# Optimization experiments

Hardware: AMD Instinct MI355X
Metric: run time of the kernel (lower is better)

## Reference

```python
import jax, jax.numpy as jnp
import numpy as np

DECAY = 0.25
THRESH = 0.4
TIME_WINDOW = 8


def act_fun(x):
    # Heaviside spike (forward of torch ActFun)
    return (x > 0.0).astype(x.dtype)


def setup_inputs() -> dict:
    key = jax.random.key(0)
    ks = jax.random.split(key, 12)
    B, C, H, W, T = 200, 2, 34, 34, TIME_WINDOW
    in_dim, h1, h2 = 2312, 800, 10
    return {
        "input": jax.random.normal(ks[0], (B, C, H, W, T), dtype=jnp.float32),
        "hebb1": jnp.zeros((in_dim, h1), dtype=jnp.float32),
        "hebb2": jnp.zeros((h1, h2), dtype=jnp.float32),
        "W1": jax.random.normal(ks[1], (h1, in_dim), dtype=jnp.float32) / np.sqrt(in_dim),
        "b1": jax.random.normal(ks[2], (h1,), dtype=jnp.float32) * 0.01,
        "W2": jax.random.normal(ks[3], (h2, h1), dtype=jnp.float32) / np.sqrt(h1),
        "b2": jax.random.normal(ks[4], (h2,), dtype=jnp.float32) * 0.01,
        "alpha1": 0.01 * jnp.ones((1,), dtype=jnp.float32),
        "alpha2": 0.01 * jnp.ones((1,), dtype=jnp.float32),
        "beta1": 0.01 * jax.random.uniform(ks[5], (1, in_dim), dtype=jnp.float32),
        "beta2": 0.01 * jax.random.uniform(ks[6], (1, h1), dtype=jnp.float32),
        "eta1": 0.1 * jax.random.uniform(ks[7], (1, h1), dtype=jnp.float32),
        "eta2": 0.1 * jax.random.uniform(ks[8], (1, h2), dtype=jnp.float32),
    }


def _mem_update(W, b, alpha, beta, eta, x, spike, mem, hebb, batch):
    # fc(x) + alpha * x @ hebb
    state = x @ W.T + b + alpha * (x @ hebb)
    mem = mem * (1.0 - spike) * DECAY + state
    now_spike = act_fun(mem - THRESH)
    # bmm of outer products then mean over batch == single GEMM / batch
    pre = x * jnp.clip(beta, 0.0, None)              # [B, in]
    post = mem / THRESH - eta                        # [B, out]
    hebb = 0.99 * hebb - (pre.T @ post) / batch      # [in, out]
    hebb = jnp.clip(hebb, -5.0, 5.0)
    return mem, now_spike, hebb


def reference(input, hebb1, hebb2, W1, b1, W2, b2, alpha1, alpha2, beta1, beta2, eta1, eta2):
    B = input.shape[0]
    T = input.shape[-1]
    xs = jnp.moveaxis(input, -1, 0).reshape(T, B, -1)  # [T, B, 2312]
    h1 = W1.shape[0]
    h2 = W2.shape[0]
    init = (
        jnp.zeros((B, h1), jnp.float32), jnp.zeros((B, h1), jnp.float32),
        jnp.zeros((B, h2), jnp.float32), jnp.zeros((B, h2), jnp.float32),
        hebb1, hebb2,
    )

    def step(carry, x):
        h1_mem, h1_spike, h2_mem, h2_spike, hb1, hb2 = carry
        h1_mem, h1_spike, hb1 = _mem_update(W1, b1, alpha1, beta1, eta1, x, h1_spike, h1_mem, hb1, B)
        h2_mem, h2_spike, hb2 = _mem_update(W2, b2, alpha2, beta2, eta2, h1_spike, h2_spike, h2_mem, hb2, B)
        return (h1_mem, h1_spike, h2_mem, h2_spike, hb1, hb2), None

    (h1_mem, h1_spike, h2_mem, h2_spike, hb1, hb2), _ = jax.lax.scan(step, init, xs)
    outs = h2_mem / THRESH
    return outs, hb1, hb2
```

## Files before the change

### kernel.cpp

```cpp
#include <hip/hip_runtime.h>

#define BATCH  200
#define IN_DIM 2312
#define HD1    800
#define HD2    10
#define TWIN   8
#define NSPLIT 8
#define KCH    304

__global__ __launch_bounds__(512) void k_transpose_in(const float* __restrict__ in,
                                                      float* __restrict__ xall) {
  __shared__ float lds[512];
  int b  = blockIdx.y;
  int i0 = blockIdx.x * 64;
  int tid = threadIdx.x;
  int il = tid >> 3, t = tid & 7;
  int i = i0 + il;
  lds[tid] = (i < IN_DIM) ? in[((size_t)(b * IN_DIM + i) << 3) + t] : 0.f;
  __syncthreads();
  int t2 = tid >> 6, il2 = tid & 63;
  int i2 = i0 + il2;
  if (i2 < IN_DIM)
    xall[((size_t)(t2 * BATCH + b)) * IN_DIM + i2] = lds[il2 * 8 + t2];
}

__global__ __launch_bounds__(256) void k_init(const float* __restrict__ h1in,
                                              const float* __restrict__ h2in,
                                              float* __restrict__ hebb1,
                                              float* __restrict__ hebb2,
                                              float* __restrict__ mem1,
                                              float* __restrict__ spike1,
                                              float* __restrict__ mem2,
                                              float* __restrict__ spike2) {
  int stride = gridDim.x * blockDim.x;
  int n1 = IN_DIM * HD1;
  for (int k = blockIdx.x * blockDim.x + threadIdx.x; k < n1; k += stride) {
    hebb1[k] = h1in[k];
    if (k < HD1 * HD2)  hebb2[k] = h2in[k];
    if (k < BATCH * HD1) { mem1[k] = 0.f; spike1[k] = 0.f; }
    if (k < BATCH * HD2) { mem2[k] = 0.f; spike2[k] = 0.f; }
  }
}

__global__ __launch_bounds__(256) void k_prep_wc1(const float* __restrict__ W1,
                                                  const float* __restrict__ hebb1,
                                                  const float* __restrict__ alpha1,
                                                  float* __restrict__ Wc1) {
  __shared__ float lds[32][33];
  float al = alpha1[0];
  int i0 = blockIdx.x * 32;
  int j0 = blockIdx.y * 32;
  int tx = threadIdx.x, ty = threadIdx.y;
#pragma unroll
  for (int q = 0; q < 4; q++) {
    int j = j0 + ty + q * 8, i = i0 + tx;
    lds[ty + q * 8][tx] = (j < HD1 && i < IN_DIM) ? W1[(size_t)j * IN_DIM + i] : 0.f;
  }
  __syncthreads();
#pragma unroll
  for (int q = 0; q < 4; q++) {
    int i = i0 + ty + q * 8, j = j0 + tx;
    if (i < IN_DIM)
      Wc1[(size_t)i * HD1 + j] = lds[tx][ty + q * 8] + al * hebb1[(size_t)i * HD1 + j];
  }
}

__global__ __launch_bounds__(256) void k_state_gemm(const float* __restrict__ xt,
                                                    const float* __restrict__ Wc1,
                                                    float* __restrict__ part) {
  __shared__ __align__(16) float As[16][68];
  __shared__ __align__(16) float Bs[16][68];
  int m0 = blockIdx.x * 64;
  int n0 = blockIdx.y * 64;
  int s  = blockIdx.z;
  int kstart = s * KCH;
  int kend   = (kstart + KCH < IN_DIM) ? kstart + KCH : IN_DIM;
  int tid = threadIdx.x;
  int tx = tid & 15, ty = tid >> 4;
  int a_m = tid >> 2;
  int a_k = (tid & 3) * 4;
  int b_k = tid >> 4;
  int b_n = (tid & 15) * 4;
  float acc[4][4] = {};
  for (int k0 = kstart; k0 < kend; k0 += 16) {
    float4 av = make_float4(0.f, 0.f, 0.f, 0.f);
    if (m0 + a_m < BATCH && k0 + a_k < kend)
      av = *(const float4*)&xt[(size_t)(m0 + a_m) * IN_DIM + k0 + a_k];
    As[a_k + 0][a_m] = av.x;
    As[a_k + 1][a_m] = av.y;
    As[a_k + 2][a_m] = av.z;
    As[a_k + 3][a_m] = av.w;
    float4 bv = make_float4(0.f, 0.f, 0.f, 0.f);
    if (k0 + b_k < kend && n0 + b_n < HD1)
      bv = *(const float4*)&Wc1[(size_t)(k0 + b_k) * HD1 + n0 + b_n];
    *(float4*)&Bs[b_k][b_n] = bv;
    __syncthreads();
#pragma unroll
    for (int kk = 0; kk < 16; kk++) {
      float4 a = *(const float4*)&As[kk][ty * 4];
      float4 b = *(const float4*)&Bs[kk][tx * 4];
      acc[0][0] += a.x * b.x; acc[0][1] += a.x * b.y; acc[0][2] += a.x * b.z; acc[0][3] += a.x * b.w;
      acc[1][0] += a.y * b.x; acc[1][1] += a.y * b.y; acc[1][2] += a.y * b.z; acc[1][3] += a.y * b.w;
      acc[2][0] += a.z * b.x; acc[2][1] += a.z * b.y; acc[2][2] += a.z * b.z; acc[2][3] += a.z * b.w;
      acc[3][0] += a.w * b.x; acc[3][1] += a.w * b.y; acc[3][2] += a.w * b.z; acc[3][3] += a.w * b.w;
    }
    __syncthreads();
  }
  int n_base = n0 + tx * 4;
  if (n_base < HD1) {
    float* pp = part + (size_t)s * BATCH * HD1;
#pragma unroll
    for (int dm = 0; dm < 4; dm++) {
      int m = m0 + ty * 4 + dm;
      if (m < BATCH)
        *(float4*)&pp[(size_t)m * HD1 + n_base] =
            make_float4(acc[dm][0], acc[dm][1], acc[dm][2], acc[dm][3]);
    }
  }
}

__global__ __launch_bounds__(256) void k_state_epi(const float* __restrict__ part,
                                                   const float* __restrict__ b1,
                                                   const float* __restrict__ eta1,
                                                   float* __restrict__ mem1,
                                                   float* __restrict__ spike1,
                                                   float* __restrict__ post1) {
  int g = blockIdx.x * blockDim.x + threadIdx.x;
  if (g >= BATCH * (HD1 / 4)) return;
  int m  = g / (HD1 / 4);
  int n4 = (g % (HD1 / 4)) * 4;
  size_t idx = (size_t)m * HD1 + n4;
  float4 sum = *(const float4*)&part[idx];
#pragma unroll
  for (int s = 1; s < NSPLIT; s++) {
    float4 p = *(const float4*)&part[(size_t)s * BATCH * HD1 + idx];
    sum.x += p.x; sum.y += p.y; sum.z += p.z; sum.w += p.w;
  }
  float4 bb = *(const float4*)&b1[n4];
  float4 ee = *(const float4*)&eta1[n4];
  float4 mo = *(const float4*)&mem1[idx];
  float4 so = *(const float4*)&spike1[idx];
  float st[4] = {sum.x + bb.x, sum.y + bb.y, sum.z + bb.z, sum.w + bb.w};
  float mof[4] = {mo.x, mo.y, mo.z, mo.w};
  float sof[4] = {so.x, so.y, so.z, so.w};
  float eef[4] = {ee.x, ee.y, ee.z, ee.w};
  float mn[4], sp[4], po[4];
#pragma unroll
  for (int q = 0; q < 4; q++) {
    mn[q] = mof[q] * (1.f - sof[q]) * 0.25f + st[q];
    sp[q] = (mn[q] - 0.4f > 0.f) ? 1.f : 0.f;
    po[q] = mn[q] / 0.4f - eef[q];
  }
  *(float4*)&mem1[idx]   = make_float4(mn[0], mn[1], mn[2], mn[3]);
  *(float4*)&spike1[idx] = make_float4(sp[0], sp[1], sp[2], sp[3]);
  *(float4*)&post1[idx]  = make_float4(po[0], po[1], po[2], po[3]);
}

__global__ __launch_bounds__(256) void k_hebb1(const float* __restrict__ xt,
                                               const float* __restrict__ post1,
                                               const float* __restrict__ beta1,
                                               float* __restrict__ hebb1) {
  __shared__ __align__(16) float As[16][68];
  __shared__ __align__(16) float Bs[16][68];
  int i0 = blockIdx.x * 64;
  int j0 = blockIdx.y * 64;
  int tid = threadIdx.x;
  int tx = tid & 15, ty = tid >> 4;
  int l_b = tid >> 4;
  int l_c = (tid & 15) * 4;
  float acc[4][4] = {};
  for (int b0 = 0; b0 < BATCH; b0 += 16) {
    float4 av = make_float4(0.f, 0.f, 0.f, 0.f);
    if (b0 + l_b < BATCH && i0 + l_c < IN_DIM)
      av = *(const float4*)&xt[(size_t)(b0 + l_b) * IN_DIM + i0 + l_c];
    *(float4*)&As[l_b][l_c] = av;
    float4 bv = make_float4(0.f, 0.f, 0.f, 0.f);
    if (b0 + l_b < BATCH && j0 + l_c < HD1)
      bv = *(const float4*)&post1[(size_t)(b0 + l_b) * HD1 + j0 + l_c];
    *(float4*)&Bs[l_b][l_c] = bv;
    __syncthreads();
#pragma unroll
    for (int kk = 0; kk < 16; kk++) {
      float4 a = *(const float4*)&As[kk][ty * 4];
      float4 b = *(const float4*)&Bs[kk][tx * 4];
      acc[0][0] += a.x * b.x; acc[0][1] += a.x * b.y; acc[0][2] += a.x * b.z; acc[0][3] += a.x * b.w;
      acc[1][0] += a.y * b.x; acc[1][1] += a.y * b.y; acc[1][2] += a.y * b.z; acc[1][3] += a.y * b.w;
      acc[2][0] += a.z * b.x; acc[2][1] += a.z * b.y; acc[2][2] += a.z * b.z; acc[2][3] += a.z * b.w;
      acc[3][0] += a.w * b.x; acc[3][1] += a.w * b.y; acc[3][2] += a.w * b.z; acc[3][3] += a.w * b.w;
    }
    __syncthreads();
  }
  int j_base = j0 + tx * 4;
  if (j_base < HD1) {
#pragma unroll
    for (int dm = 0; dm < 4; dm++) {
      int i = i0 + ty * 4 + dm;
      if (i >= IN_DIM) continue;
      float bc = fmaxf(beta1[i], 0.f);
      size_t idx = (size_t)i * HD1 + j_base;
      float4 h = *(const float4*)&hebb1[idx];
      float hv[4] = {h.x, h.y, h.z, h.w};
#pragma unroll
      for (int dn = 0; dn < 4; dn++) {
        float v = 0.99f * hv[dn] - bc * acc[dm][dn] * (1.f / 200.f);
        hv[dn] = fminf(fmaxf(v, -5.f), 5.f);
      }
      *(float4*)&hebb1[idx] = make_float4(hv[0], hv[1], hv[2], hv[3]);
    }
  }
}

__global__ __launch_bounds__(256) void k_layer2_state(const float* __restrict__ spike1,
                                                      const float* __restrict__ W2,
                                                      const float* __restrict__ b2,
                                                      const float* __restrict__ hebb2,
                                                      const float* __restrict__ alpha2,
                                                      const float* __restrict__ eta2,
                                                      float* __restrict__ mem2,
                                                      float* __restrict__ spike2,
                                                      float* __restrict__ post2,
                                                      float* __restrict__ outs) {
  int wid  = (int)((blockIdx.x * blockDim.x + threadIdx.x) >> 6);
  int lane = threadIdx.x & 63;
  if (wid >= BATCH * HD2) return;
  int b = wid / HD2, j = wid % HD2;
  float al = alpha2[0];
  float acc = 0.f;
  for (int i = lane; i < HD1; i += 64)
    acc += spike1[b * HD1 + i] * (W2[j * HD1 + i] + al * hebb2[i * HD2 + j]);
#pragma unroll
  for (int off = 32; off > 0; off >>= 1) acc += __shfl_down(acc, off, 64);
  if (lane == 0) {
    float state = acc + b2[j];
    int idx = b * HD2 + j;
    float mo = mem2[idx], so = spike2[idx];
    float mn = mo * (1.f - so) * 0.25f + state;
    mem2[idx]   = mn;
    spike2[idx] = (mn - 0.4f > 0.f) ? 1.f : 0.f;
    post2[idx]  = mn / 0.4f - eta2[j];
    outs[idx]   = mn / 0.4f;
  }
}

__global__ __launch_bounds__(256) void k_hebb2(const float* __restrict__ spike1,
                                               const float* __restrict__ post2,
                                               const float* __restrict__ beta2,
                                               float* __restrict__ hebb2) {
  int idx = blockIdx.x * blockDim.x + threadIdx.x;
  if (idx >= HD1 * HD2) return;
  int i = idx % HD1, j = idx / HD1;
  float acc = 0.f;
  for (int b = 0; b < BATCH; b++)
    acc += spike1[b * HD1 + i] * post2[b * HD2 + j];
  float bc = fmaxf(beta2[i], 0.f);
  float h = 0.99f * hebb2[i * HD2 + j] - bc * acc * (1.f / 200.f);
  hebb2[i * HD2 + j] = fminf(fmaxf(h, -5.f), 5.f);
}

extern "C" void kernel_launch(void* const* d_in, const int* in_sizes, int n_in,
                              void* d_out, int out_size, void* d_ws, size_t ws_size,
                              hipStream_t stream) {
  const float* input    = (const float*)d_in[0];
  const float* hebb1_in = (const float*)d_in[1];
  const float* hebb2_in = (const float*)d_in[2];
  const float* W1       = (const float*)d_in[3];
  const float* b1       = (const float*)d_in[4];
  const float* W2       = (const float*)d_in[5];
  const float* b2       = (const float*)d_in[6];
  const float* alpha1   = (const float*)d_in[7];
  const float* alpha2   = (const float*)d_in[8];
  const float* beta1    = (const float*)d_in[9];
  const float* beta2    = (const float*)d_in[10];
  const float* eta1     = (const float*)d_in[11];
  const float* eta2     = (const float*)d_in[12];

  float* out   = (float*)d_out;
  float* outs  = out;
  float* hebb1 = out + BATCH * HD2;
  float* hebb2 = hebb1 + (size_t)IN_DIM * HD1;

  float* ws     = (float*)d_ws;
  float* xall   = ws;
  float* Wc1    = xall + (size_t)TWIN * BATCH * IN_DIM;
  float* part   = Wc1 + (size_t)IN_DIM * HD1;
  float* mem1   = part + (size_t)NSPLIT * BATCH * HD1;
  float* spike1 = mem1 + BATCH * HD1;
  float* post1  = spike1 + BATCH * HD1;
  float* mem2   = post1 + BATCH * HD1;
  float* spike2 = mem2 + BATCH * HD2;
  float* post2  = spike2 + BATCH * HD2;

  k_transpose_in<<<dim3((IN_DIM + 63) / 64, BATCH), 512, 0, stream>>>(input, xall);
  k_init<<<1024, 256, 0, stream>>>(hebb1_in, hebb2_in, hebb1, hebb2,
                                   mem1, spike1, mem2, spike2);

  for (int t = 0; t < TWIN; t++) {
    const float* xt = xall + (size_t)t * BATCH * IN_DIM;
    k_prep_wc1<<<dim3(73, 25), dim3(32, 8), 0, stream>>>(W1, hebb1, alpha1, Wc1);
    k_state_gemm<<<dim3(4, 13, NSPLIT), 256, 0, stream>>>(xt, Wc1, part);
    k_state_epi<<<dim3((BATCH * (HD1 / 4) + 255) / 256), 256, 0, stream>>>(
        part, b1, eta1, mem1, spike1, post1);
    k_hebb1<<<dim3(37, 13), 256, 0, stream>>>(xt, post1, beta1, hebb1);
    k_layer2_state<<<dim3((BATCH * HD2 * 64 + 255) / 256), 256, 0, stream>>>(
        spike1, W2, b2, hebb2, alpha2, eta2, mem2, spike2, post2, outs);
    k_hebb2<<<dim3((HD1 * HD2 + 255) / 256), 256, 0, stream>>>(spike1, post2, beta2, hebb2);
  }
}
```

Before: 640.9 us.

## Hoist W1 transpose and fuse alpha*hebb1 combine into state GEMM loads

W1 is now transposed once before the time loop. The per-step kernel that built the combined weight Wc1 = W1^T + alpha*hebb1 is removed; the state GEMM instead reads W1T and hebb1 directly and combines them while loading its B tile. This drops one full-matrix write and read plus a launch per timestep. The GEMM and hebb1 kernels also move to 128 threads computing 8x4 outputs each, and the split-K factor rises to 16 with shorter K chunks. The trade-off is that hebb1 is re-read by each M block, and the epilogue now sums more partial buffers.

```diff
diff --git a/kernel.cpp b/kernel.cpp
--- a/kernel.cpp
+++ b/kernel.cpp
@@ -5,8 +5,8 @@
 #define HD1    800
 #define HD2    10
 #define TWIN   8
-#define NSPLIT 8
-#define KCH    304
+#define NSPLIT 16
+#define KCH    144
 
 __global__ __launch_bounds__(512) void k_transpose_in(const float* __restrict__ in,
                                                       float* __restrict__ xall) {
@@ -22,6 +22,26 @@
   int i2 = i0 + il2;
   if (i2 < IN_DIM)
     xall[((size_t)(t2 * BATCH + b)) * IN_DIM + i2] = lds[il2 * 8 + t2];
+}
+
+__global__ __launch_bounds__(256) void k_prep_w1t(const float* __restrict__ W1,
+                                                  float* __restrict__ W1T) {
+  __shared__ float lds[32][33];
+  int i0 = blockIdx.x * 32;
+  int j0 = blockIdx.y * 32;
+  int tx = threadIdx.x, ty = threadIdx.y;
+#pragma unroll
+  for (int q = 0; q < 4; q++) {
+    int j = j0 + ty + q * 8, i = i0 + tx;
+    lds[ty + q * 8][tx] = (j < HD1 && i < IN_DIM) ? W1[(size_t)j * IN_DIM + i] : 0.f;
+  }
+  __syncthreads();
+#pragma unroll
+  for (int q = 0; q < 4; q++) {
+    int i = i0 + ty + q * 8, j = j0 + tx;
+    if (i < IN_DIM)
+      W1T[(size_t)i * HD1 + j] = lds[tx][ty + q * 8];
+  }
 }
 
 __global__ __launch_bounds__(256) void k_init(const float* __restrict__ h1in,
@@ -42,31 +62,10 @@
   }
 }
 
-__global__ __launch_bounds__(256) void k_prep_wc1(const float* __restrict__ W1,
-                                                  const float* __restrict__ hebb1,
-                                                  const float* __restrict__ alpha1,
-                                                  float* __restrict__ Wc1) {
-  __shared__ float lds[32][33];
-  float al = alpha1[0];
-  int i0 = blockIdx.x * 32;
-  int j0 = blockIdx.y * 32;
-  int tx = threadIdx.x, ty = threadIdx.y;
-#pragma unroll
-  for (int q = 0; q < 4; q++) {
-    int j = j0 + ty + q * 8, i = i0 + tx;
-    lds[ty + q * 8][tx] = (j < HD1 && i < IN_DIM) ? W1[(size_t)j * IN_DIM + i] : 0.f;
-  }
-  __syncthreads();
-#pragma unroll
-  for (int q = 0; q < 4; q++) {
-    int i = i0 + ty + q * 8, j = j0 + tx;
-    if (i < IN_DIM)
-      Wc1[(size_t)i * HD1 + j] = lds[tx][ty + q * 8] + al * hebb1[(size_t)i * HD1 + j];
-  }
-}
-
-__global__ __launch_bounds__(256) void k_state_gemm(const float* __restrict__ xt,
-                                                    const float* __restrict__ Wc1,
+__global__ __launch_bounds__(128) void k_state_gemm(const float* __restrict__ xt,
+                                                    const float* __restrict__ W1T,
+                                                    const float* __restrict__ hebb1,
+                                                    const float* __restrict__ alpha1,
                                                     float* __restrict__ part) {
   __shared__ __align__(16) float As[16][68];
   __shared__ __align__(16) float Bs[16][68];
@@ -74,35 +73,57 @@
   int n0 = blockIdx.y * 64;
   int s  = blockIdx.z;
   int kstart = s * KCH;
-  int kend   = (kstart + KCH < IN_DIM) ? kstart + KCH : IN_DIM;
+  int kend   = (s == NSPLIT - 1) ? IN_DIM : kstart + KCH;
+  float al = alpha1[0];
   int tid = threadIdx.x;
   int tx = tid & 15, ty = tid >> 4;
   int a_m = tid >> 2;
   int a_k = (tid & 3) * 4;
-  int b_k = tid >> 4;
-  int b_n = (tid & 15) * 4;
-  float acc[4][4] = {};
+  int b_k = tid >> 3;
+  int b_n = (tid & 7) * 8;
+  float acc[8][4] = {};
   for (int k0 = kstart; k0 < kend; k0 += 16) {
-    float4 av = make_float4(0.f, 0.f, 0.f, 0.f);
-    if (m0 + a_m < BATCH && k0 + a_k < kend)
-      av = *(const float4*)&xt[(size_t)(m0 + a_m) * IN_DIM + k0 + a_k];
-    As[a_k + 0][a_m] = av.x;
-    As[a_k + 1][a_m] = av.y;
-    As[a_k + 2][a_m] = av.z;
-    As[a_k + 3][a_m] = av.w;
-    float4 bv = make_float4(0.f, 0.f, 0.f, 0.f);
-    if (k0 + b_k < kend && n0 + b_n < HD1)
-      bv = *(const float4*)&Wc1[(size_t)(k0 + b_k) * HD1 + n0 + b_n];
-    *(float4*)&Bs[b_k][b_n] = bv;
+#pragma unroll
+    for (int h = 0; h < 2; h++) {
+      int m = m0 + a_m + h * 32;
+      float4 av = make_float4(0.f, 0.f, 0.f, 0.f);
+      if (m < BATCH && k0 + a_k < kend)
+        av = *(const float4*)&xt[(size_t)m * IN_DIM + k0 + a_k];
+      As[a_k + 0][a_m + h * 32] = av.x;
+      As[a_k + 1][a_m + h * 32] = av.y;
+      As[a_k + 2][a_m + h * 32] = av.z;
+      As[a_k + 3][a_m + h * 32] = av.w;
+    }
+    {
+      int kb = k0 + b_k;
+      bool kv = (kb < kend);
+      size_t base = (size_t)kb * HD1 + n0 + b_n;
+#pragma unroll
+      for (int h = 0; h < 2; h++) {
+        float4 bv = make_float4(0.f, 0.f, 0.f, 0.f);
+        if (kv && n0 + b_n + h * 4 < HD1) {
+          float4 w = *(const float4*)&W1T[base + h * 4];
+          float4 hb = *(const float4*)&hebb1[base + h * 4];
+          bv = make_float4(w.x + al * hb.x, w.y + al * hb.y,
+                           w.z + al * hb.z, w.w + al * hb.w);
+        }
+        *(float4*)&Bs[b_k][b_n + h * 4] = bv;
+      }
+    }
     __syncthreads();
 #pragma unroll
     for (int kk = 0; kk < 16; kk++) {
-      float4 a = *(const float4*)&As[kk][ty * 4];
-      float4 b = *(const float4*)&Bs[kk][tx * 4];
-      acc[0][0] += a.x * b.x; acc[0][1] += a.x * b.y; acc[0][2] += a.x * b.z; acc[0][3] += a.x * b.w;
-      acc[1][0] += a.y * b.x; acc[1][1] += a.y * b.y; acc[1][2] += a.y * b.z; acc[1][3] += a.y * b.w;
-      acc[2][0] += a.z * b.x; acc[2][1] += a.z * b.y; acc[2][2] += a.z * b.z; acc[2][3] += a.z * b.w;
-      acc[3][0] += a.w * b.x; acc[3][1] += a.w * b.y; acc[3][2] += a.w * b.z; acc[3][3] += a.w * b.w;
+      float4 a0 = *(const float4*)&As[kk][ty * 8];
+      float4 a1 = *(const float4*)&As[kk][ty * 8 + 4];
+      float4 b  = *(const float4*)&Bs[kk][tx * 4];
+      float am[8] = {a0.x, a0.y, a0.z, a0.w, a1.x, a1.y, a1.z, a1.w};
+#pragma unroll
+      for (int dm = 0; dm < 8; dm++) {
+        acc[dm][0] += am[dm] * b.x;
+        acc[dm][1] += am[dm] * b.y;
+        acc[dm][2] += am[dm] * b.z;
+        acc[dm][3] += am[dm] * b.w;
+      }
     }
     __syncthreads();
   }
@@ -110,8 +131,8 @@
   if (n_base < HD1) {
     float* pp = part + (size_t)s * BATCH * HD1;
 #pragma unroll
-    for (int dm = 0; dm < 4; dm++) {
-      int m = m0 + ty * 4 + dm;
+    for (int dm = 0; dm < 8; dm++) {
+      int m = m0 + ty * 8 + dm;
       if (m < BATCH)
         *(float4*)&pp[(size_t)m * HD1 + n_base] =
             make_float4(acc[dm][0], acc[dm][1], acc[dm][2], acc[dm][3]);
@@ -140,7 +161,7 @@
   float4 ee = *(const float4*)&eta1[n4];
   float4 mo = *(const float4*)&mem1[idx];
   float4 so = *(const float4*)&spike1[idx];
-  float st[4] = {sum.x + bb.x, sum.y + bb.y, sum.z + bb.z, sum.w + bb.w};
+  float st[4]  = {sum.x + bb.x, sum.y + bb.y, sum.z + bb.z, sum.w + bb.w};
   float mof[4] = {mo.x, mo.y, mo.z, mo.w};
   float sof[4] = {so.x, so.y, so.z, so.w};
   float eef[4] = {ee.x, ee.y, ee.z, ee.w};
@@ -156,7 +177,7 @@
   *(float4*)&post1[idx]  = make_float4(po[0], po[1], po[2], po[3]);
 }
 
-__global__ __launch_bounds__(256) void k_hebb1(const float* __restrict__ xt,
+__global__ __launch_bounds__(128) void k_hebb1(const float* __restrict__ xt,
                                                const float* __restrict__ post1,
                                                const float* __restrict__ beta1,
                                                float* __restrict__ hebb1) {
@@ -166,35 +187,45 @@
   int j0 = blockIdx.y * 64;
   int tid = threadIdx.x;
   int tx = tid & 15, ty = tid >> 4;
-  int l_b = tid >> 4;
-  int l_c = (tid & 15) * 4;
-  float acc[4][4] = {};
+  int l_b = tid >> 3;
+  int l_c = (tid & 7) * 8;
+  float acc[8][4] = {};
   for (int b0 = 0; b0 < BATCH; b0 += 16) {
-    float4 av = make_float4(0.f, 0.f, 0.f, 0.f);
-    if (b0 + l_b < BATCH && i0 + l_c < IN_DIM)
-      av = *(const float4*)&xt[(size_t)(b0 + l_b) * IN_DIM + i0 + l_c];
-    *(float4*)&As[l_b][l_c] = av;
-    float4 bv = make_float4(0.f, 0.f, 0.f, 0.f);
-    if (b0 + l_b < BATCH && j0 + l_c < HD1)
-      bv = *(const float4*)&post1[(size_t)(b0 + l_b) * HD1 + j0 + l_c];
-    *(float4*)&Bs[l_b][l_c] = bv;
+    int bb = b0 + l_b;
+    bool bv_ok = (bb < BATCH);
+#pragma unroll
+    for (int h = 0; h < 2; h++) {
+      float4 av = make_float4(0.f, 0.f, 0.f, 0.f);
+      if (bv_ok && i0 + l_c + h * 4 < IN_DIM)
+        av = *(const float4*)&xt[(size_t)bb * IN_DIM + i0 + l_c + h * 4];
+      *(float4*)&As[l_b][l_c + h * 4] = av;
+      float4 pv = make_float4(0.f, 0.f, 0.f, 0.f);
+      if (bv_ok && j0 + l_c + h * 4 < HD1)
+        pv = *(const float4*)&post1[(size_t)bb * HD1 + j0 + l_c + h * 4];
+      *(float4*)&Bs[l_b][l_c + h * 4] = pv;
+    }
     __syncthreads();
 #pragma unroll
     for (int kk = 0; kk < 16; kk++) {
-      float4 a = *(const float4*)&As[kk][ty * 4];
-      float4 b = *(const float4*)&Bs[kk][tx * 4];
-      acc[0][0] += a.x * b.x; acc[0][1] += a.x * b.y; acc[0][2] += a.x * b.z; acc[0][3] += a.x * b.w;
-      acc[1][0] += a.y * b.x; acc[1][1] += a.y * b.y; acc[1][2] += a.y * b.z; acc[1][3] += a.y * b.w;
-      acc[2][0] += a.z * b.x; acc[2][1] += a.z * b.y; acc[2][2] += a.z * b.z; acc[2][3] += a.z * b.w;
-      acc[3][0] += a.w * b.x; acc[3][1] += a.w * b.y; acc[3][2] += a.w * b.z; acc[3][3] += a.w * b.w;
+      float4 a0 = *(const float4*)&As[kk][ty * 8];
+      float4 a1 = *(const float4*)&As[kk][ty * 8 + 4];
+      float4 b  = *(const float4*)&Bs[kk][tx * 4];
+      float am[8] = {a0.x, a0.y, a0.z, a0.w, a1.x, a1.y, a1.z, a1.w};
+#pragma unroll
+      for (int dm = 0; dm < 8; dm++) {
+        acc[dm][0] += am[dm] * b.x;
+        acc[dm][1] += am[dm] * b.y;
+        acc[dm][2] += am[dm] * b.z;
+        acc[dm][3] += am[dm] * b.w;
+      }
     }
     __syncthreads();
   }
   int j_base = j0 + tx * 4;
   if (j_base < HD1) {
 #pragma unroll
-    for (int dm = 0; dm < 4; dm++) {
-      int i = i0 + ty * 4 + dm;
+    for (int dm = 0; dm < 8; dm++) {
+      int i = i0 + ty * 8 + dm;
       if (i >= IN_DIM) continue;
       float bc = fmaxf(beta1[i], 0.f);
       size_t idx = (size_t)i * HD1 + j_base;
@@ -281,8 +312,8 @@
 
   float* ws     = (float*)d_ws;
   float* xall   = ws;
-  float* Wc1    = xall + (size_t)TWIN * BATCH * IN_DIM;
-  float* part   = Wc1 + (size_t)IN_DIM * HD1;
+  float* W1T    = xall + (size_t)TWIN * BATCH * IN_DIM;
+  float* part   = W1T + (size_t)IN_DIM * HD1;
   float* mem1   = part + (size_t)NSPLIT * BATCH * HD1;
   float* spike1 = mem1 + BATCH * HD1;
   float* post1  = spike1 + BATCH * HD1;
@@ -291,16 +322,16 @@
   float* post2  = spike2 + BATCH * HD2;
 
   k_transpose_in<<<dim3((IN_DIM + 63) / 64, BATCH), 512, 0, stream>>>(input, xall);
+  k_prep_w1t<<<dim3(73, 25), dim3(32, 8), 0, stream>>>(W1, W1T);
   k_init<<<1024, 256, 0, stream>>>(hebb1_in, hebb2_in, hebb1, hebb2,
                                    mem1, spike1, mem2, spike2);
 
   for (int t = 0; t < TWIN; t++) {
     const float* xt = xall + (size_t)t * BATCH * IN_DIM;
-    k_prep_wc1<<<dim3(73, 25), dim3(32, 8), 0, stream>>>(W1, hebb1, alpha1, Wc1);
-    k_state_gemm<<<dim3(4, 13, NSPLIT), 256, 0, stream>>>(xt, Wc1, part);
+    k_state_gemm<<<dim3(4, 13, NSPLIT), 128, 0, stream>>>(xt, W1T, hebb1, alpha1, part);
     k_state_epi<<<dim3((BATCH * (HD1 / 4) + 255) / 256), 256, 0, stream>>>(
         part, b1, eta1, mem1, spike1, post1);
-    k_hebb1<<<dim3(37, 13), 256, 0, stream>>>(xt, post1, beta1, hebb1);
+    k_hebb1<<<dim3(37, 13), 256 / 2, 0, stream>>>(xt, post1, beta1, hebb1);
     k_layer2_state<<<dim3((BATCH * HD2 * 64 + 255) / 256), 256, 0, stream>>>(
         spike1, W2, b2, hebb2, alpha2, eta2, mem2, spike2, post2, outs);
     k_hebb2<<<dim3((HD1 * HD2 + 255) / 256), 256, 0, stream>>>(spike1, post2, beta2, hebb2);
```

New measurement: 700.6 us. 9.3% more time.
